# Performance work log

Measured on AMD Instinct MI355X. Metric: run time of the kernel, lower is better.

The kernel has to match this reference:

```python
import jax, jax.numpy as jnp
import numpy as np

N_IN, N_HID, HEADS = 7, 28, 7
HEAD_DIM = N_HID // HEADS  # 4
LN_EPS = 1e-5


def setup_inputs() -> dict:
    key = jax.random.key(0)
    ks = jax.random.split(key, 16)
    B, S = 16, 1024
    s_in = 1.0 / np.sqrt(N_IN)
    s_hid = 1.0 / np.sqrt(N_HID)
    inp = {
        "inputs": jax.random.normal(ks[0], (B, S, N_IN), dtype=jnp.float32),
        "Wq": jax.random.normal(ks[1], (N_IN, N_HID), dtype=jnp.float32) * s_in,
        "bq": jax.random.normal(ks[2], (N_HID,), dtype=jnp.float32) * s_in,
        "Wk": jax.random.normal(ks[3], (N_IN, N_HID), dtype=jnp.float32) * s_in,
        "bk": jax.random.normal(ks[4], (N_HID,), dtype=jnp.float32) * s_in,
        "Wv": jax.random.normal(ks[5], (N_IN, N_HID), dtype=jnp.float32) * s_in,
        "bv": jax.random.normal(ks[6], (N_HID,), dtype=jnp.float32) * s_in,
        "ln_w": jnp.ones((N_HID,), dtype=jnp.float32),
        "ln_b": jnp.zeros((N_HID,), dtype=jnp.float32),
        "W1": jax.random.normal(ks[7], (N_HID, N_IN), dtype=jnp.float32) * s_hid,
        "b1": jax.random.normal(ks[8], (N_IN,), dtype=jnp.float32) * s_hid,
        "Wq2": jax.random.normal(ks[9], (N_IN, N_HID), dtype=jnp.float32) * s_in,
        "bq2": jax.random.normal(ks[10], (N_HID,), dtype=jnp.float32) * s_in,
        "Wk2": jax.random.normal(ks[11], (N_IN, N_HID), dtype=jnp.float32) * s_in,
        "bk2": jax.random.normal(ks[12], (N_HID,), dtype=jnp.float32) * s_in,
    }
    return inp


def reference(inputs, Wq, bq, Wk, bk, Wv, bv, ln_w, ln_b, W1, b1, Wq2, bq2, Wk2, bk2):
    B, S, _ = inputs.shape
    # QKV projections -> [B, S, H, Dh]
    Q = (inputs @ Wq + bq).reshape(B, S, HEADS, HEAD_DIM)
    K = (inputs @ Wk + bk).reshape(B, S, HEADS, HEAD_DIM)
    V = (inputs @ Wv + bv).reshape(B, S, HEADS, HEAD_DIM)
    # multi-head attention, scores [B, H, Sq, Sk]
    scores = jnp.einsum("bqhd,bkhd->bhqk", Q, K) / jnp.sqrt(jnp.float32(HEAD_DIM))
    attn = jax.nn.softmax(scores, axis=-1)
    out = jnp.einsum("bhqk,bkhd->bqhd", attn, V).reshape(B, S, N_HID)
    # LayerNorm over last dim
    mu = jnp.mean(out, axis=-1, keepdims=True)
    var = jnp.var(out, axis=-1, keepdims=True)
    out = (out - mu) / jnp.sqrt(var + LN_EPS) * ln_w + ln_b
    # FFN + relu + residual
    out = jax.nn.relu(out @ W1 + b1) + inputs  # [B, S, N_IN]
    # second attention (weights only)
    Q2 = out @ Wq2 + bq2  # [B, S, N_HID]
    K2 = out @ Wk2 + bk2
    scores2 = jnp.einsum("bqh,bkh->bqk", Q2, K2) / jnp.sqrt(jnp.float32(N_IN))
    attn2 = jax.nn.softmax(scores2, axis=-1)  # [B, S, S]
    return (out, attn2)
```

## Files before the change

### kernel.cpp

```cpp
#include <hip/hip_runtime.h>

#define BB 16
#define SS 1024
#define NIN 7
#define NHID 28
#define NH 7
#define DH 4

#define EXP2F(x) __builtin_amdgcn_exp2f(x)

constexpr int ROWS = BB * SS;
constexpr int QKV_ELEMS = BB * NH * SS * DH;

__global__ __launch_bounds__(256) void k_proj(
    const float* __restrict__ inp,
    const float* __restrict__ Wq, const float* __restrict__ bq,
    const float* __restrict__ Wk, const float* __restrict__ bk,
    const float* __restrict__ Wv, const float* __restrict__ bv,
    float* __restrict__ Qo, float* __restrict__ Ko, float* __restrict__ Vo)
{
    __shared__ float  xs[256 * NIN];
    __shared__ float4 w4[147];
    __shared__ float4 b4[21];

    const int tid  = threadIdx.x;
    const int row0 = blockIdx.x * 256;

    #pragma unroll
    for (int i = 0; i < NIN; ++i) xs[tid + 256 * i] = inp[row0 * NIN + tid + 256 * i];

    if (tid < 147) {
        const float* src = (tid < 49) ? Wq : (tid < 98) ? Wk : Wv;
        int off = (tid < 49) ? tid : (tid < 98) ? tid - 49 : tid - 98;
        w4[tid] = ((const float4*)src)[off];
    } else if (tid < 168) {
        int t = tid - 147;
        const float* src = (t < 7) ? bq : (t < 14) ? bk : bv;
        b4[t] = ((const float4*)src)[t % 7];
    }
    __syncthreads();

    const int r = row0 + tid;
    const int b = r >> 10, s = r & 1023;

    float x[NIN];
    #pragma unroll
    for (int i = 0; i < NIN; ++i) x[i] = xs[tid * NIN + i];

    float4 q[NH], k[NH], v[NH];
    #pragma unroll
    for (int j4 = 0; j4 < NH; ++j4) { q[j4] = b4[j4]; k[j4] = b4[7 + j4]; v[j4] = b4[14 + j4]; }

    #pragma unroll
    for (int i = 0; i < NIN; ++i) {
        const float xi = x[i];
        #pragma unroll
        for (int j4 = 0; j4 < NH; ++j4) {
            float4 wq = w4[i * 7 + j4];
            float4 wk = w4[49 + i * 7 + j4];
            float4 wv = w4[98 + i * 7 + j4];
            q[j4].x += xi * wq.x; q[j4].y += xi * wq.y; q[j4].z += xi * wq.z; q[j4].w += xi * wq.w;
            k[j4].x += xi * wk.x; k[j4].y += xi * wk.y; k[j4].z += xi * wk.z; k[j4].w += xi * wk.w;
            v[j4].x += xi * wv.x; v[j4].y += xi * wv.y; v[j4].z += xi * wv.z; v[j4].w += xi * wv.w;
        }
    }

    const float qs_scale = 0.5f * 1.4426950408889634f;
    #pragma unroll
    for (int j4 = 0; j4 < NH; ++j4) {
        const int idx = (b * NH + j4) * SS + s;
        float4 qs = make_float4(qs_scale * q[j4].x, qs_scale * q[j4].y,
                                qs_scale * q[j4].z, qs_scale * q[j4].w);
        ((float4*)Qo)[idx] = qs;
        ((float4*)Ko)[idx] = k[j4];
        ((float4*)Vo)[idx] = v[j4];
    }
}

__global__ __launch_bounds__(512) void k_attn1(
    const float* __restrict__ Qo, const float* __restrict__ Ko,
    const float* __restrict__ Vo, float* __restrict__ A)
{
    __shared__ char smem[40960];
    float4* Ksh  = (float4*)smem;
    float4* Vsh  = (float4*)(smem + 16384);
    float4* pacc = (float4*)smem;
    float*  pl   = (float*)(smem + 32768);

    const int bh  = blockIdx.x >> 2;
    const int qt  = blockIdx.x & 3;
    const int tid = threadIdx.x;

    const float4* Kg = (const float4*)Ko + (size_t)bh * SS;
    const float4* Vg = (const float4*)Vo + (size_t)bh * SS;
    #pragma unroll
    for (int i = 0; i < 2; ++i) {
        Ksh[tid + 512 * i] = Kg[tid + 512 * i];
        Vsh[tid + 512 * i] = Vg[tid + 512 * i];
    }
    __syncthreads();

    const int ql = tid & 63;
    const int kq = tid >> 6;

    float4 qv[4];
    #pragma unroll
    for (int r = 0; r < 4; ++r)
        qv[r] = ((const float4*)Qo)[(size_t)bh * SS + qt * 256 + r * 64 + ql];

    float4 acc[4];
    float  l[4];
    #pragma unroll
    for (int r = 0; r < 4; ++r) { acc[r] = make_float4(0.f, 0.f, 0.f, 0.f); l[r] = 0.f; }

    const int k0 = kq << 7;
    #pragma unroll 4
    for (int kk = k0; kk < k0 + 128; ++kk) {
        float4 kr = Ksh[kk];
        float4 vr = Vsh[kk];
        #pragma unroll
        for (int r = 0; r < 4; ++r) {
            float s = qv[r].x * kr.x + qv[r].y * kr.y + qv[r].z * kr.z + qv[r].w * kr.w;
            float p = EXP2F(s);
            l[r] += p;
            acc[r].x += p * vr.x; acc[r].y += p * vr.y;
            acc[r].z += p * vr.z; acc[r].w += p * vr.w;
        }
    }

    __syncthreads();
    #pragma unroll
    for (int r = 0; r < 4; ++r) {
        pacc[kq * 256 + r * 64 + ql] = acc[r];
        pl[kq * 256 + r * 64 + ql]   = l[r];
    }
    __syncthreads();

    if (tid < 256) {
        float4 a  = pacc[tid];
        float  ll = pl[tid];
        #pragma unroll
        for (int j = 1; j < 8; ++j) {
            float4 t = pacc[j * 256 + tid];
            a.x += t.x; a.y += t.y; a.z += t.z; a.w += t.w;
            ll += pl[j * 256 + tid];
        }
        const float inv = 1.f / ll;
        const int b = bh / NH, h = bh % NH;
        const int q = qt * 256 + tid;
        ((float4*)A)[(size_t)(b * SS + q) * NH + h] =
            make_float4(a.x * inv, a.y * inv, a.z * inv, a.w * inv);
    }
}

__global__ __launch_bounds__(256) void k_lnffn(
    const float* __restrict__ A, const float* __restrict__ inp,
    const float* __restrict__ lnw, const float* __restrict__ lnb,
    const float* __restrict__ W1, const float* __restrict__ b1,
    const float* __restrict__ Wq2, const float* __restrict__ bq2,
    const float* __restrict__ Wk2, const float* __restrict__ bk2,
    float* __restrict__ outp, float* __restrict__ Q2, float* __restrict__ K2T)
{
    const int r = blockIdx.x * 256 + threadIdx.x;

    float y[NHID];
    const float4* Ar = (const float4*)A + (size_t)r * 7;
    float mu = 0.f;
    #pragma unroll
    for (int j4 = 0; j4 < 7; ++j4) {
        float4 t = Ar[j4];
        y[4 * j4 + 0] = t.x; y[4 * j4 + 1] = t.y; y[4 * j4 + 2] = t.z; y[4 * j4 + 3] = t.w;
        mu += t.x + t.y + t.z + t.w;
    }
    mu *= (1.f / NHID);
    float var = 0.f;
    #pragma unroll
    for (int j = 0; j < NHID; ++j) { float d = y[j] - mu; var += d * d; }
    var *= (1.f / NHID);
    const float rstd = rsqrtf(var + 1e-5f);
    #pragma unroll
    for (int j = 0; j < NHID; ++j) y[j] = (y[j] - mu) * rstd * lnw[j] + lnb[j];

    float o[NIN];
    #pragma unroll
    for (int i = 0; i < NIN; ++i) {
        float a = b1[i];
        #pragma unroll
        for (int j = 0; j < NHID; ++j) a += y[j] * W1[j * NIN + i];
        o[i] = fmaxf(a, 0.f) + inp[r * NIN + i];
        outp[r * NIN + i] = o[i];
    }

    const float rs7l2e = 0.3779644730092272f * 1.4426950408889634f;
    const int b = r >> 10, s = r & 1023;
    float* K2Tb = K2T + ((size_t)b * NHID) * SS + s;
    float4* Q2r = (float4*)Q2 + (size_t)r * 7;
    #pragma unroll
    for (int j4 = 0; j4 < 7; ++j4) {
        float qq[4];
        #pragma unroll
        for (int c = 0; c < 4; ++c) {
            int j = 4 * j4 + c;
            float aq = bq2[j], ak = bk2[j];
            #pragma unroll
            for (int i = 0; i < NIN; ++i) {
                aq += o[i] * Wq2[i * NHID + j];
                ak += o[i] * Wk2[i * NHID + j];
            }
            qq[c] = aq * rs7l2e;
            K2Tb[(size_t)j * SS] = ak;
        }
        Q2r[j4] = make_float4(qq[0], qq[1], qq[2], qq[3]);
    }
}

#define QR 4
__global__ __launch_bounds__(256, 4) void k_attn2(
    const float* __restrict__ Q2, const float* __restrict__ K2T,
    float* __restrict__ out2)
{
    __shared__ float q2s[16 * NHID];

    const int tid  = threadIdx.x;
    const int lane = tid & 63;
    const int wid  = tid >> 6;
    const int row0 = blockIdx.x * 16;
    const int b    = row0 >> 10;

    if (tid < 112) ((float4*)q2s)[tid] = ((const float4*)Q2)[(size_t)row0 * 7 + tid];
    __syncthreads();

    const float*  qw  = q2s + wid * QR * NHID;
    const float4* K2b = (const float4*)(K2T + (size_t)b * NHID * SS);

    float4 p0[QR], p1[QR], p2[QR], p3[QR];
    #pragma unroll
    for (int r = 0; r < QR; ++r) {
        p0[r] = make_float4(0.f, 0.f, 0.f, 0.f);
        p1[r] = make_float4(0.f, 0.f, 0.f, 0.f);
        p2[r] = make_float4(0.f, 0.f, 0.f, 0.f);
        p3[r] = make_float4(0.f, 0.f, 0.f, 0.f);
    }

    #pragma unroll 2
    for (int d = 0; d < NHID; ++d) {
        float4 kt0 = K2b[d * 256 +       lane];
        float4 kt1 = K2b[d * 256 +  64 + lane];
        float4 kt2 = K2b[d * 256 + 128 + lane];
        float4 kt3 = K2b[d * 256 + 192 + lane];
        #pragma unroll
        for (int r = 0; r < QR; ++r) {
            const float qd = qw[r * NHID + d];
            p0[r].x += qd * kt0.x; p0[r].y += qd * kt0.y;
            p0[r].z += qd * kt0.z; p0[r].w += qd * kt0.w;
            p1[r].x += qd * kt1.x; p1[r].y += qd * kt1.y;
            p1[r].z += qd * kt1.z; p1[r].w += qd * kt1.w;
            p2[r].x += qd * kt2.x; p2[r].y += qd * kt2.y;
            p2[r].z += qd * kt2.z; p2[r].w += qd * kt2.w;
            p3[r].x += qd * kt3.x; p3[r].y += qd * kt3.y;
            p3[r].z += qd * kt3.z; p3[r].w += qd * kt3.w;
        }
    }

    #pragma unroll
    for (int r = 0; r < QR; ++r) {
        p0[r].x = EXP2F(p0[r].x); p0[r].y = EXP2F(p0[r].y);
        p0[r].z = EXP2F(p0[r].z); p0[r].w = EXP2F(p0[r].w);
        p1[r].x = EXP2F(p1[r].x); p1[r].y = EXP2F(p1[r].y);
        p1[r].z = EXP2F(p1[r].z); p1[r].w = EXP2F(p1[r].w);
        p2[r].x = EXP2F(p2[r].x); p2[r].y = EXP2F(p2[r].y);
        p2[r].z = EXP2F(p2[r].z); p2[r].w = EXP2F(p2[r].w);
        p3[r].x = EXP2F(p3[r].x); p3[r].y = EXP2F(p3[r].y);
        p3[r].z = EXP2F(p3[r].z); p3[r].w = EXP2F(p3[r].w);
        float sum = p0[r].x + p0[r].y + p0[r].z + p0[r].w
                  + p1[r].x + p1[r].y + p1[r].z + p1[r].w
                  + p2[r].x + p2[r].y + p2[r].z + p2[r].w
                  + p3[r].x + p3[r].y + p3[r].z + p3[r].w;
        #pragma unroll
        for (int off = 1; off < 64; off <<= 1) sum += __shfl_xor(sum, off);
        const float iv = 1.f / sum;
        float4* orow = (float4*)(out2 + ((size_t)row0 + wid * QR + r) * SS);
        orow[       lane] = make_float4(p0[r].x * iv, p0[r].y * iv, p0[r].z * iv, p0[r].w * iv);
        orow[ 64 + lane] = make_float4(p1[r].x * iv, p1[r].y * iv, p1[r].z * iv, p1[r].w * iv);
        orow[128 + lane] = make_float4(p2[r].x * iv, p2[r].y * iv, p2[r].z * iv, p2[r].w * iv);
        orow[192 + lane] = make_float4(p3[r].x * iv, p3[r].y * iv, p3[r].z * iv, p3[r].w * iv);
    }
}

extern "C" void kernel_launch(void* const* d_in, const int* in_sizes, int n_in,
                              void* d_out, int out_size, void* d_ws, size_t ws_size,
                              hipStream_t stream) {
    const float* inp = (const float*)d_in[0];
    const float* Wq  = (const float*)d_in[1];
    const float* bq  = (const float*)d_in[2];
    const float* Wk  = (const float*)d_in[3];
    const float* bk  = (const float*)d_in[4];
    const float* Wv  = (const float*)d_in[5];
    const float* bv  = (const float*)d_in[6];
    const float* lnw = (const float*)d_in[7];
    const float* lnb = (const float*)d_in[8];
    const float* W1  = (const float*)d_in[9];
    const float* b1  = (const float*)d_in[10];
    const float* Wq2 = (const float*)d_in[11];
    const float* bq2 = (const float*)d_in[12];
    const float* Wk2 = (const float*)d_in[13];
    const float* bk2 = (const float*)d_in[14];

    float* out0 = (float*)d_out;
    float* out2 = out0 + ROWS * NIN;

    float* ws = (float*)d_ws;
    float* Qo  = ws;
    float* Ko  = ws + (size_t)QKV_ELEMS;
    float* Vo  = ws + (size_t)2 * QKV_ELEMS;
    float* A   = ws + (size_t)3 * QKV_ELEMS;
    float* Q2  = ws + (size_t)4 * QKV_ELEMS;
    float* K2T = ws + (size_t)5 * QKV_ELEMS;

    k_proj <<<ROWS / 256, 256, 0, stream>>>(inp, Wq, bq, Wk, bk, Wv, bv, Qo, Ko, Vo);
    k_attn1<<<BB * NH * 4, 512, 0, stream>>>(Qo, Ko, Vo, A);
    k_lnffn<<<ROWS / 256, 256, 0, stream>>>(A, inp, lnw, lnb, W1, b1,
                                            Wq2, bq2, Wk2, bk2, out0, Q2, K2T);
    k_attn2<<<ROWS / 16, 256, 0, stream>>>(Q2, K2T, out2);
}
```

Measured before the change: 183.2 us.

## Split attention-1 over key chunks and reduce partials in LN/FFN kernel

The first attention kernel now splits the key dimension into four chunks, launching four times as many blocks that each process 256 keys and write unnormalized partial accumulators and softmax denominators. The LayerNorm/FFN kernel sums the four partials per head and normalizes before LayerNorm. This increases parallelism and reduces per-block serial work, and temporarily reuses the second attention's output buffer as scratch. It adds extra global traffic for the partial results.

```diff
diff --git a/kernel.cpp b/kernel.cpp
--- a/kernel.cpp
+++ b/kernel.cpp
@@ -11,6 +11,7 @@
 
 constexpr int ROWS = BB * SS;
 constexpr int QKV_ELEMS = BB * NH * SS * DH;
+constexpr int CHUNK_STRIDE = BB * NH * SS;
 
 __global__ __launch_bounds__(256) void k_proj(
     const float* __restrict__ inp,
@@ -79,26 +80,24 @@
 
 __global__ __launch_bounds__(512) void k_attn1(
     const float* __restrict__ Qo, const float* __restrict__ Ko,
-    const float* __restrict__ Vo, float* __restrict__ A)
+    const float* __restrict__ Vo, float4* __restrict__ Apart,
+    float* __restrict__ Lpart)
 {
     __shared__ char smem[40960];
     float4* Ksh  = (float4*)smem;
-    float4* Vsh  = (float4*)(smem + 16384);
+    float4* Vsh  = (float4*)(smem + 4096);
     float4* pacc = (float4*)smem;
     float*  pl   = (float*)(smem + 32768);
 
-    const int bh  = blockIdx.x >> 2;
-    const int qt  = blockIdx.x & 3;
+    const int bh  = blockIdx.x >> 4;
+    const int qt  = (blockIdx.x >> 2) & 3;
+    const int ks  = blockIdx.x & 3;
     const int tid = threadIdx.x;
 
-    const float4* Kg = (const float4*)Ko + (size_t)bh * SS;
-    const float4* Vg = (const float4*)Vo + (size_t)bh * SS;
-    #pragma unroll
-    for (int i = 0; i < 2; ++i) {
-        Ksh[tid + 512 * i] = Kg[tid + 512 * i];
-        Vsh[tid + 512 * i] = Vg[tid + 512 * i];
-    }
-    __syncthreads();
+    const float4* Kg = (const float4*)Ko + (size_t)bh * SS + (ks << 8);
+    const float4* Vg = (const float4*)Vo + (size_t)bh * SS + (ks << 8);
+    if (tid < 256) Ksh[tid]       = Kg[tid];
+    else           Vsh[tid - 256] = Vg[tid - 256];
 
     const int ql = tid & 63;
     const int kq = tid >> 6;
@@ -106,16 +105,18 @@
     float4 qv[4];
     #pragma unroll
     for (int r = 0; r < 4; ++r)
-        qv[r] = ((const float4*)Qo)[(size_t)bh * SS + qt * 256 + r * 64 + ql];
+        qv[r] = ((const float4*)Qo)[(size_t)bh * SS + (qt << 8) + r * 64 + ql];
+
+    __syncthreads();
 
     float4 acc[4];
     float  l[4];
     #pragma unroll
     for (int r = 0; r < 4; ++r) { acc[r] = make_float4(0.f, 0.f, 0.f, 0.f); l[r] = 0.f; }
 
-    const int k0 = kq << 7;
+    const int k0 = kq << 5;
     #pragma unroll 4
-    for (int kk = k0; kk < k0 + 128; ++kk) {
+    for (int kk = k0; kk < k0 + 32; ++kk) {
         float4 kr = Ksh[kk];
         float4 vr = Vsh[kk];
         #pragma unroll
@@ -145,16 +146,15 @@
             a.x += t.x; a.y += t.y; a.z += t.z; a.w += t.w;
             ll += pl[j * 256 + tid];
         }
-        const float inv = 1.f / ll;
-        const int b = bh / NH, h = bh % NH;
-        const int q = qt * 256 + tid;
-        ((float4*)A)[(size_t)(b * SS + q) * NH + h] =
-            make_float4(a.x * inv, a.y * inv, a.z * inv, a.w * inv);
+        const size_t o = ((size_t)(ks * (BB * NH) + bh) << 10) + (qt << 8) + tid;
+        Apart[o] = a;
+        Lpart[o] = ll;
     }
 }
 
 __global__ __launch_bounds__(256) void k_lnffn(
-    const float* __restrict__ A, const float* __restrict__ inp,
+    const float4* __restrict__ Apart, const float* __restrict__ Lpart,
+    const float* __restrict__ inp,
     const float* __restrict__ lnw, const float* __restrict__ lnb,
     const float* __restrict__ W1, const float* __restrict__ b1,
     const float* __restrict__ Wq2, const float* __restrict__ bq2,
@@ -162,15 +162,25 @@
     float* __restrict__ outp, float* __restrict__ Q2, float* __restrict__ K2T)
 {
     const int r = blockIdx.x * 256 + threadIdx.x;
+    const int b = r >> 10, s = r & 1023;
 
     float y[NHID];
-    const float4* Ar = (const float4*)A + (size_t)r * 7;
     float mu = 0.f;
     #pragma unroll
-    for (int j4 = 0; j4 < 7; ++j4) {
-        float4 t = Ar[j4];
-        y[4 * j4 + 0] = t.x; y[4 * j4 + 1] = t.y; y[4 * j4 + 2] = t.z; y[4 * j4 + 3] = t.w;
-        mu += t.x + t.y + t.z + t.w;
+    for (int h = 0; h < NH; ++h) {
+        const size_t base = ((size_t)(b * NH + h) << 10) + s;
+        float4 a  = Apart[base];
+        float  ll = Lpart[base];
+        #pragma unroll
+        for (int c = 1; c < 4; ++c) {
+            float4 t = Apart[base + (size_t)c * CHUNK_STRIDE];
+            a.x += t.x; a.y += t.y; a.z += t.z; a.w += t.w;
+            ll += Lpart[base + (size_t)c * CHUNK_STRIDE];
+        }
+        const float inv = 1.f / ll;
+        y[4 * h + 0] = a.x * inv; y[4 * h + 1] = a.y * inv;
+        y[4 * h + 2] = a.z * inv; y[4 * h + 3] = a.w * inv;
+        mu += (a.x + a.y + a.z + a.w) * inv;
     }
     mu *= (1.f / NHID);
     float var = 0.f;
@@ -192,7 +202,6 @@
     }
 
     const float rs7l2e = 0.3779644730092272f * 1.4426950408889634f;
-    const int b = r >> 10, s = r & 1023;
     float* K2Tb = K2T + ((size_t)b * NHID) * SS + s;
     float4* Q2r = (float4*)Q2 + (size_t)r * 7;
     #pragma unroll
@@ -309,17 +318,19 @@
     float* out0 = (float*)d_out;
     float* out2 = out0 + ROWS * NIN;
 
+    float4* Apart = (float4*)out2;
+    float*  Lpart = out2 + (size_t)4 * QKV_ELEMS;
+
     float* ws = (float*)d_ws;
     float* Qo  = ws;
     float* Ko  = ws + (size_t)QKV_ELEMS;
     float* Vo  = ws + (size_t)2 * QKV_ELEMS;
-    float* A   = ws + (size_t)3 * QKV_ELEMS;
-    float* Q2  = ws + (size_t)4 * QKV_ELEMS;
-    float* K2T = ws + (size_t)5 * QKV_ELEMS;
+    float* Q2  = ws + (size_t)3 * QKV_ELEMS;
+    float* K2T = ws + (size_t)4 * QKV_ELEMS;
 
     k_proj <<<ROWS / 256, 256, 0, stream>>>(inp, Wq, bq, Wk, bk, Wv, bv, Qo, Ko, Vo);
-    k_attn1<<<BB * NH * 4, 512, 0, stream>>>(Qo, Ko, Vo, A);
-    k_lnffn<<<ROWS / 256, 256, 0, stream>>>(A, inp, lnw, lnb, W1, b1,
+    k_attn1<<<BB * NH * 16, 512, 0, stream>>>(Qo, Ko, Vo, Apart, Lpart);
+    k_lnffn<<<ROWS / 256, 256, 0, stream>>>(Apart, Lpart, inp, lnw, lnb, W1, b1,
                                             Wq2, bq2, Wk2, bk2, out0, Q2, K2T);
     k_attn2<<<ROWS / 16, 256, 0, stream>>>(Q2, K2T, out2);
 }
```

After: 175.6 us. 4.2% less time.
